# Optimization experiments

Measured on AMD Instinct MI355X. Metric: run time of the kernel, lower is better.

The kernel has to match this reference:

```python
import jax, jax.numpy as jnp
import numpy as np

N = 500_000        # atoms
P = 16_000_000     # neighbor pairs (half list)
NS = 4             # species types
CUTOFF = 2.5
BOX = 20.0         # cubic box edge length


def setup_inputs() -> dict:
    key = jax.random.key(0)
    k = jax.random.split(key, 6)
    positions = jax.random.uniform(k[0], (N, 3), dtype=jnp.float32) * BOX
    cell = jnp.eye(3, dtype=jnp.float32) * BOX
    pair_i = jax.random.randint(k[1], (P,), 0, N, dtype=jnp.int32)
    # guarantee j != i so r2 > 0 even when shift == 0
    offs = jax.random.randint(k[2], (P,), 1, N, dtype=jnp.int32)
    pair_j = (pair_i + offs) % N
    shifts = jax.random.randint(k[3], (P, 3), 0, 3, dtype=jnp.int32)
    species = jax.random.randint(k[4], (N,), 0, NS, dtype=jnp.int32)
    # per-species-pair LJ parameter tables (symmetric), mirroring the
    # dict {(a,b): (sigma, epsilon)} precomputation in __init__
    sig = 0.8 + 0.1 * jnp.arange(NS, dtype=jnp.float32)
    eps = 0.5 + 0.1 * jnp.arange(NS, dtype=jnp.float32)
    sigma_tab = 0.5 * (sig[:, None] + sig[None, :])
    eps_tab = jnp.sqrt(eps[:, None] * eps[None, :])
    sr = sigma_tab / CUTOFF
    shift_tab = 4.0 * eps_tab * (sr ** 12 - sr ** 6)
    return dict(positions=positions, cell=cell, sigma_tab=sigma_tab,
                eps_tab=eps_tab, shift_tab=shift_tab, species=species,
                pair_i=pair_i, pair_j=pair_j, shifts=shifts)


def reference(positions, cell, sigma_tab, eps_tab, shift_tab,
              species, pair_i, pair_j, shifts):
    # gather species-pair params (vectorized dict lookup)
    si = species[pair_i]
    sj = species[pair_j]
    sigma = sigma_tab[si, sj]        # [P]
    epsilon = eps_tab[si, sj]        # [P]
    shift_e = shift_tab[si, sj]      # [P]
    # displacement with periodic cell shift: r_j - r_i + S @ cell
    d = positions[pair_j] - positions[pair_i] + shifts.astype(positions.dtype) @ cell  # [P,3]
    r2 = jnp.sum(d * d, axis=-1)     # [P]
    r6 = r2 * r2 * r2
    sigma3 = sigma * sigma * sigma
    sigma6 = sigma3 * sigma3
    sr6 = sigma6 / r6
    sr12 = sr6 * sr6
    e = 4.0 * epsilon * (sr12 - sr6) - shift_e   # [P]
    # per-atom energy: half to each endpoint (per_atom=True path)
    energy = jnp.zeros(positions.shape[0], dtype=positions.dtype)
    energy = energy.at[pair_i].add(0.5 * e).at[pair_j].add(0.5 * e)
    return energy
```

## Files before the change

### kernel.cpp

```cpp
#include <hip/hip_runtime.h>


#define BUCKET_SHIFT 11
#define BUCKET_SIZE  2048
#define SLICES       8
#define QSCALE       2048.0f
#define QINV         (1.0f / 2048.0f)

__global__ void lj_zero_kernel(float* __restrict__ out, long n) {
    long i = (long)blockIdx.x * blockDim.x + threadIdx.x;
    if (i < n) out[i] = 0.0f;
}

__global__ void lj_pack8_kernel(const float* __restrict__ pos,
                                const int* __restrict__ species,
                                unsigned long long* __restrict__ tab8,
                                int* __restrict__ cursor,
                                int nb, int cap, int n) {
    int i = blockIdx.x * blockDim.x + threadIdx.x;
    if (i < n) {
        unsigned int ux = (unsigned int)(pos[3 * i]     * QSCALE + 0.5f) & 0xFFFFu;
        unsigned int uy = (unsigned int)(pos[3 * i + 1] * QSCALE + 0.5f) & 0xFFFFu;
        unsigned int uz = (unsigned int)(pos[3 * i + 2] * QSCALE + 0.5f) & 0xFFFFu;
        unsigned long long w = (unsigned long long)ux
                             | ((unsigned long long)uy << 16)
                             | ((unsigned long long)uz << 32)
                             | ((unsigned long long)(species[i] & 3) << 48);
        tab8[i] = w;
    }
    if (i < nb) cursor[i] = i * cap;
}

__global__ void lj_pack_kernel(const float* __restrict__ pos,
                               const int* __restrict__ species,
                               float4* __restrict__ packed, int n) {
    int i = blockIdx.x * blockDim.x + threadIdx.x;
    if (i < n) {
        float4 p;
        p.x = pos[3 * i];
        p.y = pos[3 * i + 1];
        p.z = pos[3 * i + 2];
        p.w = __int_as_float(species[i]);
        packed[i] = p;
    }
}

__device__ __forceinline__ unsigned int lj_encode(float he) {
    unsigned int u = __float_as_uint(he);
    return (u + 0x400u) & 0xFFFFF800u;
}

__global__ __launch_bounds__(1024) void lj_passA_kernel(
    const unsigned long long* __restrict__ tab8,
    const float* __restrict__ cell,
    const float* __restrict__ sigma_tab,
    const float* __restrict__ eps_tab,
    const float* __restrict__ shift_tab,
    const int* __restrict__ pair_i,
    const int* __restrict__ pair_j,
    const int* __restrict__ shifts,
    unsigned int* __restrict__ record_buf,
    int* __restrict__ cursor,
    int cap, int nb, int P)
{
    __shared__ float s_sig6[16];
    __shared__ float s_eps4[16];
    __shared__ float s_shift[16];
    __shared__ float s_cell[9];
    __shared__ int hist[256];
    __shared__ int basev[256];
    int t = threadIdx.x;
    if (t < 16) {
        float s = sigma_tab[t];
        float s3 = s * s * s;
        s_sig6[t] = s3 * s3;
        s_eps4[t] = 4.0f * eps_tab[t];
        s_shift[t] = shift_tab[t];
    }
    if (t < 9) s_cell[t] = cell[t];
    if (t < 256) hist[t] = 0;
    __syncthreads();

    float c00 = s_cell[0], c01 = s_cell[1], c02 = s_cell[2];
    float c10 = s_cell[3], c11 = s_cell[4], c12 = s_cell[5];
    float c20 = s_cell[6], c21 = s_cell[7], c22 = s_cell[8];

    long base = (long)(blockIdx.x * (long)blockDim.x + t) * 4;

    int   ai[4], aj[4];
    float hev[4];
    int   sloti[4], slotj[4];
    bool  valid[4];

    if (base + 3 < P) {
        int4 pi4 = *(const int4*)(pair_i + base);
        int4 pj4 = *(const int4*)(pair_j + base);
        int4 sA = *(const int4*)(shifts + base * 3);
        int4 sB = *(const int4*)(shifts + base * 3 + 4);
        int4 sC = *(const int4*)(shifts + base * 3 + 8);
        int pis[4] = {pi4.x, pi4.y, pi4.z, pi4.w};
        int pjs[4] = {pj4.x, pj4.y, pj4.z, pj4.w};
        int shv[12] = {sA.x, sA.y, sA.z, sA.w, sB.x, sB.y, sB.z, sB.w,
                       sC.x, sC.y, sC.z, sC.w};
#pragma unroll
        for (int k = 0; k < 4; ++k) {
            int i = pis[k], j = pjs[k];
            float fx = (float)shv[3 * k], fy = (float)shv[3 * k + 1], fz = (float)shv[3 * k + 2];
            unsigned long long gi = tab8[i];
            unsigned long long gj = tab8[j];
            int xi = (int)(gi & 0xFFFFu), yi = (int)((gi >> 16) & 0xFFFFu), zi = (int)((gi >> 32) & 0xFFFFu);
            int xj = (int)(gj & 0xFFFFu), yj = (int)((gj >> 16) & 0xFFFFu), zj = (int)((gj >> 32) & 0xFFFFu);
            float dlx = (float)(xj - xi) * QINV;
            float dly = (float)(yj - yi) * QINV;
            float dlz = (float)(zj - zi) * QINV;
            float dx = dlx + fx * c00 + fy * c10 + fz * c20;
            float dy = dly + fx * c01 + fy * c11 + fz * c21;
            float dz = dlz + fx * c02 + fy * c12 + fz * c22;
            float r2 = dx * dx + dy * dy + dz * dz;
            float r6 = r2 * r2 * r2;
            int idx = (int)(gi >> 48) * 4 + (int)(gj >> 48);
            float sr6 = s_sig6[idx] / r6;
            float sr12 = sr6 * sr6;
            hev[k] = 0.5f * (s_eps4[idx] * (sr12 - sr6) - s_shift[idx]);
            ai[k] = i; aj[k] = j; valid[k] = true;
        }
    } else {
#pragma unroll
        for (int k = 0; k < 4; ++k) {
            long p = base + k;
            valid[k] = (p < P);
            ai[k] = 0; aj[k] = 0; hev[k] = 0.0f;
            if (valid[k]) {
                int i = pair_i[p], j = pair_j[p];
                float fx = (float)shifts[3 * p], fy = (float)shifts[3 * p + 1], fz = (float)shifts[3 * p + 2];
                unsigned long long gi = tab8[i];
                unsigned long long gj = tab8[j];
                int xi = (int)(gi & 0xFFFFu), yi = (int)((gi >> 16) & 0xFFFFu), zi = (int)((gi >> 32) & 0xFFFFu);
                int xj = (int)(gj & 0xFFFFu), yj = (int)((gj >> 16) & 0xFFFFu), zj = (int)((gj >> 32) & 0xFFFFu);
                float dlx = (float)(xj - xi) * QINV;
                float dly = (float)(yj - yi) * QINV;
                float dlz = (float)(zj - zi) * QINV;
                float dx = dlx + fx * c00 + fy * c10 + fz * c20;
                float dy = dly + fx * c01 + fy * c11 + fz * c21;
                float dz = dlz + fx * c02 + fy * c12 + fz * c22;
                float r2 = dx * dx + dy * dy + dz * dz;
                float r6 = r2 * r2 * r2;
                int idx = (int)(gi >> 48) * 4 + (int)(gj >> 48);
                float sr6 = s_sig6[idx] / r6;
                float sr12 = sr6 * sr6;
                hev[k] = 0.5f * (s_eps4[idx] * (sr12 - sr6) - s_shift[idx]);
                ai[k] = i; aj[k] = j;
            }
        }
    }

#pragma unroll
    for (int k = 0; k < 4; ++k) {
        if (valid[k]) {
            sloti[k] = atomicAdd(&hist[ai[k] >> BUCKET_SHIFT], 1);
            slotj[k] = atomicAdd(&hist[aj[k] >> BUCKET_SHIFT], 1);
        } else {
            sloti[k] = 0; slotj[k] = 0;
        }
    }
    __syncthreads();

    if (t < nb) {
        int h = hist[t];
        basev[t] = (h > 0) ? atomicAdd(&cursor[t], h) : 0;
    }
    __syncthreads();

#pragma unroll
    for (int k = 0; k < 4; ++k) {
        if (valid[k]) {
            unsigned int u = lj_encode(hev[k]);
            int bi = ai[k] >> BUCKET_SHIFT;
            int wi = basev[bi] + sloti[k];
            if (wi < (bi + 1) * cap)
                record_buf[wi] = u | (unsigned int)(ai[k] & (BUCKET_SIZE - 1));
            int bj = aj[k] >> BUCKET_SHIFT;
            int wj = basev[bj] + slotj[k];
            if (wj < (bj + 1) * cap)
                record_buf[wj] = u | (unsigned int)(aj[k] & (BUCKET_SIZE - 1));
        }
    }
}

__global__ __launch_bounds__(256) void lj_passB_kernel(
    const unsigned int* __restrict__ record_buf,
    const int* __restrict__ cursor,
    float* __restrict__ partial,
    int cap)
{
    __shared__ float e[BUCKET_SIZE];
    int blk = blockIdx.x;
    int b = blk >> 3;
    int s = blk & (SLICES - 1);
    int t = threadIdx.x;
#pragma unroll
    for (int k = 0; k < 8; ++k) e[t + 256 * k] = 0.0f;
    __syncthreads();

    int begin = b * cap;
    int count = cursor[b] - begin;
    if (count > cap) count = cap;

    int ngroups = (count + 7) >> 3;
    int gps = (ngroups + SLICES - 1) / SLICES;
    int g0 = s * gps;
    int g1 = g0 + gps;
    if (g1 > ngroups) g1 = ngroups;

    for (int g = g0 + t; g < g1; g += 256) {
        int r0 = g * 8;
        const unsigned int* rp = record_buf + begin + r0;
        if (r0 + 8 <= count) {
            int4 a = *(const int4*)(rp);
            int4 c = *(const int4*)(rp + 4);
            unsigned int w0 = (unsigned int)a.x, w1 = (unsigned int)a.y;
            unsigned int w2 = (unsigned int)a.z, w3 = (unsigned int)a.w;
            unsigned int w4 = (unsigned int)c.x, w5 = (unsigned int)c.y;
            unsigned int w6 = (unsigned int)c.z, w7 = (unsigned int)c.w;
            atomicAdd(&e[w0 & 2047u], __uint_as_float(w0 & 0xFFFFF800u));
            atomicAdd(&e[w1 & 2047u], __uint_as_float(w1 & 0xFFFFF800u));
            atomicAdd(&e[w2 & 2047u], __uint_as_float(w2 & 0xFFFFF800u));
            atomicAdd(&e[w3 & 2047u], __uint_as_float(w3 & 0xFFFFF800u));
            atomicAdd(&e[w4 & 2047u], __uint_as_float(w4 & 0xFFFFF800u));
            atomicAdd(&e[w5 & 2047u], __uint_as_float(w5 & 0xFFFFF800u));
            atomicAdd(&e[w6 & 2047u], __uint_as_float(w6 & 0xFFFFF800u));
            atomicAdd(&e[w7 & 2047u], __uint_as_float(w7 & 0xFFFFF800u));
        } else {
            for (int r = r0; r < count; ++r) {
                unsigned int w = record_buf[begin + r];
                atomicAdd(&e[w & 2047u], __uint_as_float(w & 0xFFFFF800u));
            }
        }
    }
    __syncthreads();

    float* pb = partial + (long)blk * BUCKET_SIZE;
#pragma unroll
    for (int k = 0; k < 8; ++k) pb[t + 256 * k] = e[t + 256 * k];
}

__global__ void lj_reduce_kernel(const float* __restrict__ partial,
                                 float* __restrict__ energy, int N) {
    int i = blockIdx.x * blockDim.x + threadIdx.x;
    if (i < N) {
        int b = i >> BUCKET_SHIFT;
        int l = i & (BUCKET_SIZE - 1);
        const float* pb = partial + ((long)b * SLICES) * BUCKET_SIZE + l;
        float s = 0.0f;
#pragma unroll
        for (int k = 0; k < SLICES; ++k) s += pb[(long)k * BUCKET_SIZE];
        energy[i] = s;
    }
}

__device__ __forceinline__ void lj_one_pair_packed(
    int i, int j, float fx, float fy, float fz,
    const float4* __restrict__ packed,
    const float* s_sig6, const float* s_eps4, const float* s_shift,
    float c00, float c01, float c02,
    float c10, float c11, float c12,
    float c20, float c21, float c22,
    float* __restrict__ energy)
{
    float4 gi = packed[i];
    float4 gj = packed[j];
    float dx = gj.x - gi.x + fx * c00 + fy * c10 + fz * c20;
    float dy = gj.y - gi.y + fx * c01 + fy * c11 + fz * c21;
    float dz = gj.z - gi.z + fx * c02 + fy * c12 + fz * c22;
    float r2 = dx * dx + dy * dy + dz * dz;
    float r6 = r2 * r2 * r2;
    int idx = __float_as_int(gi.w) * 4 + __float_as_int(gj.w);
    float sr6 = s_sig6[idx] / r6;
    float sr12 = sr6 * sr6;
    float he = 0.5f * (s_eps4[idx] * (sr12 - sr6) - s_shift[idx]);
    atomicAdd(energy + i, he);
    atomicAdd(energy + j, he);
}

__global__ __launch_bounds__(256) void lj_pairs_packed_kernel(
    const float4* __restrict__ packed,
    const float* __restrict__ cell,
    const float* __restrict__ sigma_tab,
    const float* __restrict__ eps_tab,
    const float* __restrict__ shift_tab,
    const int* __restrict__ pair_i,
    const int* __restrict__ pair_j,
    const int* __restrict__ shifts,
    float* __restrict__ energy,
    int P)
{
    __shared__ float s_sig6[16];
    __shared__ float s_eps4[16];
    __shared__ float s_shift[16];
    __shared__ float s_cell[9];
    int t = threadIdx.x;
    if (t < 16) {
        float s = sigma_tab[t];
        float s3 = s * s * s;
        s_sig6[t] = s3 * s3;
        s_eps4[t] = 4.0f * eps_tab[t];
        s_shift[t] = shift_tab[t];
    }
    if (t < 9) s_cell[t] = cell[t];
    __syncthreads();

    float c00 = s_cell[0], c01 = s_cell[1], c02 = s_cell[2];
    float c10 = s_cell[3], c11 = s_cell[4], c12 = s_cell[5];
    float c20 = s_cell[6], c21 = s_cell[7], c22 = s_cell[8];

    long base = (long)(blockIdx.x * (long)blockDim.x + t) * 4;
    if (base + 3 < P) {
        int4 pi4 = *(const int4*)(pair_i + base);
        int4 pj4 = *(const int4*)(pair_j + base);
        int4 sA = *(const int4*)(shifts + base * 3);
        int4 sB = *(const int4*)(shifts + base * 3 + 4);
        int4 sC = *(const int4*)(shifts + base * 3 + 8);
        int pis[4] = {pi4.x, pi4.y, pi4.z, pi4.w};
        int pjs[4] = {pj4.x, pj4.y, pj4.z, pj4.w};
        int shv[12] = {sA.x, sA.y, sA.z, sA.w, sB.x, sB.y, sB.z, sB.w,
                       sC.x, sC.y, sC.z, sC.w};
#pragma unroll
        for (int k = 0; k < 4; ++k) {
            lj_one_pair_packed(pis[k], pjs[k],
                        (float)shv[3 * k], (float)shv[3 * k + 1], (float)shv[3 * k + 2],
                        packed, s_sig6, s_eps4, s_shift,
                        c00, c01, c02, c10, c11, c12, c20, c21, c22, energy);
        }
    } else {
        for (long p = base; p < P; ++p) {
            lj_one_pair_packed(pair_i[p], pair_j[p],
                        (float)shifts[3 * p], (float)shifts[3 * p + 1], (float)shifts[3 * p + 2],
                        packed, s_sig6, s_eps4, s_shift,
                        c00, c01, c02, c10, c11, c12, c20, c21, c22, energy);
        }
    }
}

__device__ __forceinline__ void lj_one_pair(
    int i, int j, float fx, float fy, float fz,
    const float* __restrict__ pos,
    const int* __restrict__ species,
    const float* s_sig6, const float* s_eps4, const float* s_shift,
    float c00, float c01, float c02,
    float c10, float c11, float c12,
    float c20, float c21, float c22,
    float* __restrict__ energy)
{
    float dx = pos[3 * j]     - pos[3 * i]     + fx * c00 + fy * c10 + fz * c20;
    float dy = pos[3 * j + 1] - pos[3 * i + 1] + fx * c01 + fy * c11 + fz * c21;
    float dz = pos[3 * j + 2] - pos[3 * i + 2] + fx * c02 + fy * c12 + fz * c22;
    float r2 = dx * dx + dy * dy + dz * dz;
    float r6 = r2 * r2 * r2;
    int idx = species[i] * 4 + species[j];
    float sr6 = s_sig6[idx] / r6;
    float sr12 = sr6 * sr6;
    float he = 0.5f * (s_eps4[idx] * (sr12 - sr6) - s_shift[idx]);
    atomicAdd(energy + i, he);
    atomicAdd(energy + j, he);
}

__global__ __launch_bounds__(256) void lj_pairs_kernel(
    const float* __restrict__ pos,
    const float* __restrict__ cell,
    const float* __restrict__ sigma_tab,
    const float* __restrict__ eps_tab,
    const float* __restrict__ shift_tab,
    const int* __restrict__ species,
    const int* __restrict__ pair_i,
    const int* __restrict__ pair_j,
    const int* __restrict__ shifts,
    float* __restrict__ energy,
    int P)
{
    __shared__ float s_sig6[16];
    __shared__ float s_eps4[16];
    __shared__ float s_shift[16];
    __shared__ float s_cell[9];
    int t = threadIdx.x;
    if (t < 16) {
        float s = sigma_tab[t];
        float s3 = s * s * s;
        s_sig6[t] = s3 * s3;
        s_eps4[t] = 4.0f * eps_tab[t];
        s_shift[t] = shift_tab[t];
    }
    if (t < 9) s_cell[t] = cell[t];
    __syncthreads();

    float c00 = s_cell[0], c01 = s_cell[1], c02 = s_cell[2];
    float c10 = s_cell[3], c11 = s_cell[4], c12 = s_cell[5];
    float c20 = s_cell[6], c21 = s_cell[7], c22 = s_cell[8];

    long base = (long)(blockIdx.x * (long)blockDim.x + t) * 4;
    if (base + 3 < P) {
        int4 pi4 = *(const int4*)(pair_i + base);
        int4 pj4 = *(const int4*)(pair_j + base);
        int4 sA = *(const int4*)(shifts + base * 3);
        int4 sB = *(const int4*)(shifts + base * 3 + 4);
        int4 sC = *(const int4*)(shifts + base * 3 + 8);
        int pis[4] = {pi4.x, pi4.y, pi4.z, pi4.w};
        int pjs[4] = {pj4.x, pj4.y, pj4.z, pj4.w};
        int shv[12] = {sA.x, sA.y, sA.z, sA.w, sB.x, sB.y, sB.z, sB.w,
                       sC.x, sC.y, sC.z, sC.w};
#pragma unroll
        for (int k = 0; k < 4; ++k) {
            lj_one_pair(pis[k], pjs[k],
                        (float)shv[3 * k], (float)shv[3 * k + 1], (float)shv[3 * k + 2],
                        pos, species, s_sig6, s_eps4, s_shift,
                        c00, c01, c02, c10, c11, c12, c20, c21, c22, energy);
        }
    } else {
        for (long p = base; p < P; ++p) {
            lj_one_pair(pair_i[p], pair_j[p],
                        (float)shifts[3 * p], (float)shifts[3 * p + 1], (float)shifts[3 * p + 2],
                        pos, species, s_sig6, s_eps4, s_shift,
                        c00, c01, c02, c10, c11, c12, c20, c21, c22, energy);
        }
    }
}

extern "C" void kernel_launch(void* const* d_in, const int* in_sizes, int n_in,
                              void* d_out, int out_size, void* d_ws, size_t ws_size,
                              hipStream_t stream) {
    const float* positions = (const float*)d_in[0];
    const float* cell      = (const float*)d_in[1];
    const float* sigma_tab = (const float*)d_in[2];
    const float* eps_tab   = (const float*)d_in[3];
    const float* shift_tab = (const float*)d_in[4];
    const int*   species   = (const int*)d_in[5];
    const int*   pair_i    = (const int*)d_in[6];
    const int*   pair_j    = (const int*)d_in[7];
    const int*   shifts    = (const int*)d_in[8];
    float* energy = (float*)d_out;

    const int N = out_size;
    const int P = in_sizes[6];

    const int threads = 256;
    const int ablocks = (N + threads - 1) / threads;
    const int pblocks4 = (int)((((long)P + 3) / 4 + threads - 1) / threads);

    const int nb = (N + BUCKET_SIZE - 1) / BUCKET_SIZE;
    long avg = (2L * P) / (nb > 0 ? nb : 1);
    long capl = (avg + avg / 50 + 512 + 1023) & ~1023L;
    const int cap = (int)capl;
    const size_t rec_bytes  = (size_t)nb * (size_t)cap * 4u;
    const size_t tab_bytes  = (size_t)N * 8u;
    const size_t cur_bytes  = (size_t)nb * 4u;
    const size_t part_bytes = (size_t)nb * SLICES * BUCKET_SIZE * 4u;
    const size_t need_bucket = rec_bytes + tab_bytes + cur_bytes + part_bytes;
    const size_t need_pack   = (size_t)N * 16u;

    const bool has_ws = (d_ws != nullptr);
    const bool sane = (nb > 0) && (nb <= 256) && ((long)nb * cap < 2000000000L);
    const bool use_bucket = has_ws && sane && (ws_size >= need_bucket);
    const bool use_pack   = has_ws && !use_bucket && (ws_size >= need_pack);

    if (use_bucket) {
        unsigned int* record_buf = (unsigned int*)d_ws;
        unsigned long long* tab8 = (unsigned long long*)((char*)d_ws + rec_bytes);
        int* cursor = (int*)((char*)d_ws + rec_bytes + tab_bytes);
        float* partial = (float*)((char*)d_ws + rec_bytes + tab_bytes + cur_bytes);

        lj_pack8_kernel<<<ablocks, threads, 0, stream>>>(
            positions, species, tab8, cursor, nb, cap, N);
        const int athreads = 1024;
        const long nthreads_needed = ((long)P + 3) / 4;
        const int pblocksA = (int)((nthreads_needed + athreads - 1) / athreads);
        lj_passA_kernel<<<pblocksA, athreads, 0, stream>>>(
            tab8, cell, sigma_tab, eps_tab, shift_tab,
            pair_i, pair_j, shifts, record_buf, cursor, cap, nb, P);
        lj_passB_kernel<<<nb * SLICES, threads, 0, stream>>>(record_buf, cursor, partial, cap);
        lj_reduce_kernel<<<ablocks, threads, 0, stream>>>(partial, energy, N);
    } else if (use_pack) {
        float4* packed = (float4*)d_ws;
        lj_zero_kernel<<<ablocks, threads, 0, stream>>>(energy, N);
        lj_pack_kernel<<<ablocks, threads, 0, stream>>>(positions, species, packed, N);
        lj_pairs_packed_kernel<<<pblocks4, threads, 0, stream>>>(
            packed, cell, sigma_tab, eps_tab, shift_tab,
            pair_i, pair_j, shifts, energy, P);
    } else {
        lj_zero_kernel<<<ablocks, threads, 0, stream>>>(energy, N);
        lj_pairs_kernel<<<pblocks4, threads, 0, stream>>>(
            positions, cell, sigma_tab, eps_tab, shift_tab, species,
            pair_i, pair_j, shifts, energy, P);
    }
}
```

Before: 821.4 us.

## Stage bucketed records in shared memory for coalesced global scatter

Pass A now computes a block-local exclusive prefix sum over bucket histograms and writes each record into a shared-memory staging array sorted by bucket. After a barrier, threads copy the staged records out contiguously per bucket, so global writes land in consecutive addresses instead of scattered per-thread stores. This costs about 40KB of extra shared memory per block, which can reduce occupancy, plus an extra barrier and a copy loop.

```diff
diff --git a/kernel.cpp b/kernel.cpp
--- a/kernel.cpp
+++ b/kernel.cpp
@@ -69,6 +69,9 @@
     __shared__ float s_cell[9];
     __shared__ int hist[256];
     __shared__ int basev[256];
+    __shared__ int bbase[256];
+    __shared__ unsigned int staged[8192];
+    __shared__ unsigned char bucketOf[8192];
     int t = threadIdx.x;
     if (t < 16) {
         float s = sigma_tab[t];
@@ -165,6 +168,22 @@
     }
     __syncthreads();
 
+    if (t < 64) {
+        int b0 = t * 4;
+        int h0 = hist[b0], h1 = hist[b0 + 1], h2 = hist[b0 + 2], h3 = hist[b0 + 3];
+        int s = h0 + h1 + h2 + h3;
+        int incl = s;
+#pragma unroll
+        for (int d = 1; d < 64; d <<= 1) {
+            int v = __shfl_up(incl, d, 64);
+            if (t >= d) incl += v;
+        }
+        int excl = incl - s;
+        bbase[b0]     = excl;
+        bbase[b0 + 1] = excl + h0;
+        bbase[b0 + 2] = excl + h0 + h1;
+        bbase[b0 + 3] = excl + h0 + h1 + h2;
+    }
     if (t < nb) {
         int h = hist[t];
         basev[t] = (h > 0) ? atomicAdd(&cursor[t], h) : 0;
@@ -176,14 +195,22 @@
         if (valid[k]) {
             unsigned int u = lj_encode(hev[k]);
             int bi = ai[k] >> BUCKET_SHIFT;
-            int wi = basev[bi] + sloti[k];
-            if (wi < (bi + 1) * cap)
-                record_buf[wi] = u | (unsigned int)(ai[k] & (BUCKET_SIZE - 1));
+            int li = bbase[bi] + sloti[k];
+            staged[li] = u | (unsigned int)(ai[k] & (BUCKET_SIZE - 1));
+            bucketOf[li] = (unsigned char)bi;
             int bj = aj[k] >> BUCKET_SHIFT;
-            int wj = basev[bj] + slotj[k];
-            if (wj < (bj + 1) * cap)
-                record_buf[wj] = u | (unsigned int)(aj[k] & (BUCKET_SIZE - 1));
-        }
+            int lidxj = bbase[bj] + slotj[k];
+            staged[lidxj] = u | (unsigned int)(aj[k] & (BUCKET_SIZE - 1));
+            bucketOf[lidxj] = (unsigned char)bj;
+        }
+    }
+    __syncthreads();
+
+    int total = bbase[255] + hist[255];
+    for (int idx = t; idx < total; idx += 1024) {
+        int b = (int)bucketOf[idx];
+        int g = basev[b] + (idx - bbase[b]);
+        if (g < (b + 1) * cap) record_buf[g] = staged[idx];
     }
 }
 
```

After: 752.6 us. 8.4% less time.
